# Performance work log

Hardware: AMD Instinct MI355X
Metric: run time of the kernel (lower is better)

The kernel has to match this reference:

```python
import jax, jax.numpy as jnp
import numpy as np

L = 1024   # latent_size
K = 8
R = L // K # 128 reduced dim
T = 32     # caption length
B = 64     # batch (images and captions)
DIN = 300  # word embedding dim
REG = 36   # image regions
R3 = 3 * R
H3 = 3 * L

def _p(key, shape, scale=0.05):
    return scale * jax.random.normal(key, shape, dtype=jnp.float32)

def setup_inputs():
    ks = jax.random.split(jax.random.key(0), 40)
    return {
        'img_embed': jax.random.normal(ks[0], (B, REG, L), jnp.float32),
        'cap_embed': jax.random.normal(ks[1], (B, T, DIN), jnp.float32),
        'lens': jax.random.randint(ks[2], (B,), 1, T + 1),
        'W_reduce_img': _p(ks[3], (R, L)), 'b_reduce_img': _p(ks[4], (R,)),
        'W_reduce_txt': _p(ks[5], (R, DIN)), 'b_reduce_txt': _p(ks[6], (R,)),
        'gru_Wih_f': _p(ks[7], (H3, DIN)), 'gru_Whh_f': _p(ks[8], (H3, L)),
        'gru_bih_f': _p(ks[9], (H3,)), 'gru_bhh_f': _p(ks[10], (H3,)),
        'gru_Wih_b': _p(ks[11], (H3, DIN)), 'gru_Whh_b': _p(ks[12], (H3, L)),
        'gru_bih_b': _p(ks[13], (H3,)), 'gru_bhh_b': _p(ks[14], (H3,)),
        'sa_Wq': _p(ks[15], (R, L)), 'sa_bq': _p(ks[16], (R,)),
        'sa_Wk': _p(ks[17], (R, L)), 'sa_bk': _p(ks[18], (R,)),
        'sa_Wv': _p(ks[19], (L, L)), 'sa_bv': _p(ks[20], (L,)),
        'sa_gamma': jnp.float32(0.5),
        'gen_Wih': _p(ks[21], (R3 * R, R)), 'gen_bih': _p(ks[22], (R3 * R,)),
        'gen_Whh': _p(ks[23], (R3 * R, R)), 'gen_bhh': _p(ks[24], (R3 * R,)),
        'gen_Wbih': _p(ks[25], (R3, R)), 'gen_bbih': _p(ks[26], (R3,)),
        'gen_Wbhh': _p(ks[27], (R3, R)), 'gen_bbhh': _p(ks[28], (R3,)),
        'W_txt_fc': _p(ks[29], (L, R + L)), 'b_txt_fc': _p(ks[30], (L,)),
    }

def l2norm(x, axis=-1, eps=1e-8):
    return x / (jnp.linalg.norm(x, axis=axis, keepdims=True) + eps)

def gru_dir(x, Wih, Whh, bih, bhh, reverse=False):
    # torch GRU math, gate order [r, z, n]; x: (B, T, D) -> (B, T, H)
    H = Whh.shape[1]
    gi = jnp.einsum('btd,hd->tbh', x, Wih) + bih  # precompute input gates (T, B, 3H)
    h0 = jnp.zeros((x.shape[0], H), x.dtype)
    def step(h, gi_t):
        gh = h @ Whh.T + bhh
        r = jax.nn.sigmoid(gi_t[:, :H] + gh[:, :H])
        z = jax.nn.sigmoid(gi_t[:, H:2 * H] + gh[:, H:2 * H])
        n = jnp.tanh(gi_t[:, 2 * H:] + r * gh[:, 2 * H:])
        hn = (1.0 - z) * n + z * h
        return hn, hn
    _, hs = jax.lax.scan(step, h0, gi, reverse=reverse)
    return jnp.swapaxes(hs, 0, 1)

def _forward(img_embed, cap_embed, lens, W_reduce_img, b_reduce_img, W_reduce_txt, b_reduce_txt,
             gru_Wih_f, gru_Whh_f, gru_bih_f, gru_bhh_f, gru_Wih_b, gru_Whh_b, gru_bih_b, gru_bhh_b,
             sa_Wq, sa_bq, sa_Wk, sa_bk, sa_Wv, sa_bv, sa_gamma,
             gen_Wih, gen_bih, gen_Whh, gen_bhh, gen_Wbih, gen_bbih, gen_Wbhh, gen_bbhh,
             W_txt_fc, b_txt_fc):
    # 1. bidirectional GRU over captions, average the two directions
    hf = gru_dir(cap_embed, gru_Wih_f, gru_Whh_f, gru_bih_f, gru_bhh_f, False)
    hb = gru_dir(cap_embed, gru_Wih_b, gru_Whh_b, gru_bih_b, gru_bhh_b, True)
    txt = (hf + hb) / 2.0                                   # (B, T, L)
    # 2. SAGAN-style 1D self-attention on (B, L, T)
    x = jnp.swapaxes(txt, 1, 2)                             # (B, L, T)
    q = jnp.einsum('bct,oc->bto', x, sa_Wq) + sa_bq          # (B, T, R)
    kk = jnp.einsum('bct,oc->bot', x, sa_Wk) + sa_bk[:, None]  # (B, R, T)
    attn = jax.nn.softmax(jnp.einsum('bto,bos->bts', q, kk), axis=-1)  # (B, T, T)
    v = jnp.einsum('bct,oc->bot', x, sa_Wv) + sa_bv[:, None]  # (B, L, T)
    x = sa_gamma * jnp.einsum('bcs,bts->bct', v, attn) + x
    # 3. length-masked mean pooling
    txt = jnp.swapaxes(x, 1, 2)                             # (B, T, L)
    mask = (jnp.arange(T)[None, :] < lens[:, None]).astype(txt.dtype)
    txt_embed = (txt * mask[:, :, None]).sum(1) / lens[:, None].astype(txt.dtype)  # (B, L)
    # 4. conv1d(k=1) reductions == linear over channel dim
    img = jnp.swapaxes(img_embed, 1, 2)                     # (B, L, REG)
    img_embed_global = img.mean(-1)                         # (B, L)
    cap_reduced = jnp.einsum('btd,od->btd2'.replace('d2','o'), cap_embed, W_reduce_txt) + b_reduce_txt  # (B, T, R)
    img_reduced = jnp.einsum('bcr,oc->bor', img, W_reduce_img) + b_reduce_img[:, None]  # (B, R, REG)
    img_global_vec = img_reduced.mean(-1)                   # (B, R)
    # 5. per-image generated-weight GRU over all captions (vmap replaces B-loop)
    def per_image(base, img_glob):
        Wih = (gen_Wih @ base + gen_bih).reshape(R3, R)
        Whh = (gen_Whh @ base + gen_bhh).reshape(R3, R)
        bih = gen_Wbih @ base + gen_bbih
        bhh = gen_Wbhh @ base + gen_bbhh
        gi = jnp.einsum('btd,hd->tbh', cap_reduced, Wih) + bih  # (T, B, 3R)
        h0 = jnp.zeros((cap_reduced.shape[0], R), cap_reduced.dtype)
        def step(h, gi_t):
            gh = h @ Whh.T + bhh
            r = jax.nn.sigmoid(gi_t[:, :R] + gh[:, :R])
            z = jax.nn.sigmoid(gi_t[:, R:2 * R] + gh[:, R:2 * R])
            n = jnp.tanh(gi_t[:, 2 * R:] + r * gh[:, 2 * R:])
            hn = (1.0 - z) * n + z * h
            return hn, hn
        _, hs = jax.lax.scan(step, h0, gi)                  # (T, B, R)
        txt_vec = hs.max(0)                                 # max over time -> (B, R)
        txt_vec = jnp.concatenate([txt_embed, txt_vec], axis=1) @ W_txt_fc.T + b_txt_fc
        txt_vec = l2norm(txt_vec)                           # (B, L)
        iv = l2norm(img_glob)                               # (L,)
        return txt_vec @ iv                                 # (B,) cosine sims for this image
    sims = jax.vmap(per_image)(img_global_vec, img_embed_global)  # (B_img, B_cap)
    return sims

def reference(img_embed, cap_embed, lens, W_reduce_img, b_reduce_img, W_reduce_txt, b_reduce_txt,
              gru_Wih_f, gru_Whh_f, gru_bih_f, gru_bhh_f, gru_Wih_b, gru_Whh_b, gru_bih_b, gru_bhh_b,
              sa_Wq, sa_bq, sa_Wk, sa_bk, sa_Wv, sa_bv, sa_gamma,
              gen_Wih, gen_bih, gen_Whh, gen_bhh, gen_Wbih, gen_bbih, gen_Wbhh, gen_bbhh,
              W_txt_fc, b_txt_fc):
    return _forward(img_embed, cap_embed, lens, W_reduce_img, b_reduce_img, W_reduce_txt, b_reduce_txt,
                    gru_Wih_f, gru_Whh_f, gru_bih_f, gru_bhh_f, gru_Wih_b, gru_Whh_b, gru_bih_b, gru_bhh_b,
                    sa_Wq, sa_bq, sa_Wk, sa_bk, sa_Wv, sa_bv, sa_gamma,
                    gen_Wih, gen_bih, gen_Whh, gen_bhh, gen_Wbih, gen_bbih, gen_Wbhh, gen_bbhh,
                    W_txt_fc, b_txt_fc)
```

## Files before the change

kernel.cpp:

```cpp
#include <hip/hip_runtime.h>
#include <math.h>

#define Lsz   1024
#define Tsz   32
#define Bsz   64
#define DIN   300
#define REG   36
#define Rsz   128
#define R3sz  384
#define H3sz  3072
#define GENROWS 49152
#define NC    2048
#define KPAD  304

typedef __attribute__((ext_vector_type(8))) short bf16x8;
typedef __attribute__((ext_vector_type(4))) float f32x4;

__device__ __forceinline__ float sigf(float x) { return 1.f / (1.f + __expf(-x)); }

__device__ __forceinline__ ushort f2bf(float x) {
    unsigned u = __float_as_uint(x);
    unsigned r = (u + 0x7fffu + ((u >> 16) & 1u)) >> 16;
    return (ushort)r;
}
// ... 311 lines not shown
    int ctp = blockIdx.x;
    int col = ctp * 16 + (l & 15);
    int kb = kt * 32 + (l >> 4) * 8;
    float v[8];
#pragma unroll
    for (int e = 0; e < 8; e++)
        v[e] = capT2[(size_t)(kb + e) * NC + col];
    size_t off = ((size_t)kt * 128 + ctp) * 512 + l * 8;
    pack8(v, (ushort*)CFh_ + off, (ushort*)CFl_ + off);
}

__global__ __launch_bounds__(256) void packwih_kernel(
    const float* __restrict__ Wf, const float* __restrict__ Wb,
    float* __restrict__ Fh, float* __restrict__ Fl)
{
    int tid = threadIdx.x, l = tid & 63, wid = tid >> 6;
    int kt = blockIdx.x * 4 + wid;
    int m = blockIdx.y, dir = blockIdx.z;
    if (kt >= 10) return;
    const float* W = dir ? Wb : Wf;
    int row = m * 16 + (l & 15);
    int kb = kt * 32 + (l >> 4) * 8;
    float v[8];
#pragma unroll
    for (int e = 0; e < 8; e++) {
        int k = kb + e;
        v[e] = (k < DIN) ? W[(size_t)row * DIN + k] : 0.f;
    }
    size_t off = (((size_t)dir * 192 + m) * 10 + kt) * 512 + l * 8;
    pack8(v, (ushort*)Fh + off, (ushort*)Fl + off);
}

__global__ __launch_bounds__(256) void packcapb_kernel(
    const float* __restrict__ cap_embed, float* __restrict__ Fh, float* __restrict__ Fl)
{
    int tid = threadIdx.x, l = tid & 63, wid = tid >> 6;
    int ct = blockIdx.x;
    int kt = blockIdx.y * 4 + wid;
    if (kt >= 10) return;
    int c = ct * 16 + (l & 15), t = c >> 6, b = c & 63;
    int kb = kt * 32 + (l >> 4) * 8;
    float v[8];
#pragma unroll
    for (int e = 0; e < 8; e++) {
        int k = kb + e;
        v[e] = (k < DIN) ? cap_embed[((size_t)b * Tsz + t) * DIN + k] : 0.f;
    }
    size_t off = ((size_t)kt * 128 + ct) * 512 + l * 8;
    pack8(v, (ushort*)Fh + off, (ushort*)Fl + off);
}

__global__ __launch_bounds__(256) void packA_rm(
    const float* __restrict__ W, float* __restrict__ Fh, float* __restrict__ Fl,
    int lda, int koff, int NKT)
{
    int tid = threadIdx.x, l = tid & 63, wid = tid >> 6;
    int strip = blockIdx.x;
    int kt = blockIdx.y * 4 + wid;
    if (kt >= NKT) return;
    int row = strip * 16 + (l & 15);
    int kb = kt * 32 + (l >> 4) * 8;
    float v[8];
    *(float4*)&v[0] = *(const float4*)&W[(size_t)row * lda + koff + kb];
    *(float4*)&v[4] = *(const float4*)&W[(size_t)row * lda + koff + kb + 4];
    size_t off = ((size_t)strip * NKT + kt) * 512 + l * 8;
    pack8(v, (ushort*)Fh + off, (ushort*)Fl + off);
}

__global__ __launch_bounds__(256) void packB_kernel(
    const float* __restrict__ X, float* __restrict__ Fh, float* __restrict__ Fl,
    int ncols, int NKT)
{
    int tid = threadIdx.x, l = tid & 63, wid = tid >> 6;
    int ctp = blockIdx.x;
    int kt = blockIdx.y * 4 + wid;
    if (kt >= NKT) return;
    int col = ctp * 16 + (l & 15);
    int kb = kt * 32 + (l >> 4) * 8;
    float v[8];
#pragma unroll
    for (int e = 0; e < 8; e++)
        v[e] = X[(size_t)(kb + e) * ncols + col];
    size_t off = ((size_t)kt * (ncols >> 4) + ctp) * 512 + l * 8;
    pack8(v, (ushort*)Fh + off, (ushort*)Fl + off);
}

__global__ __launch_bounds__(256) void gemm_mfma(
    const float* __restrict__ AFh, const float* __restrict__ AFl,
    const float* __restrict__ BFh, const float* __restrict__ BFl,
    const float* __restrict__ bias, float* __restrict__ C,
    int NKT, int ncols)
{
    __shared__ __align__(16) ushort BsH[8][512];
    __shared__ __align__(16) ushort BsL[8][512];
    int tid = threadIdx.x, l = tid & 63, wid = tid >> 6;
    int ctg = blockIdx.x, mg = blockIdx.y;
    int ct0 = ctg * 8;
    int m0 = mg * 8 + wid * 2;
    int nct = ncols >> 4;
    const ushort* AH = (const ushort*)AFh;
    const ushort* AL = (const ushort*)AFl;
    const ushort* BH = (const ushort*)BFh;
    const ushort* BL = (const ushort*)BFl;

    f32x4 acc[2][8];
#pragma unroll
    for (int m = 0; m < 2; m++)
#pragma unroll
        for (int ct = 0; ct < 8; ct++) acc[m][ct] = (f32x4){0.f, 0.f, 0.f, 0.f};

    for (int kt = 0; kt < NKT; kt++) {
        __syncthreads();
#pragma unroll
        for (int u = 0; u < 2; u++) {
            int e = u * 256 + tid;
            int ct = e >> 6, p8 = (e & 63) * 8;
            *(uint4*)&BsH[ct][p8] = *(const uint4*)&BH[((size_t)kt * nct + ct0 + ct) * 512 + p8];
            *(uint4*)&BsL[ct][p8] = *(const uint4*)&BL[((size_t)kt * nct + ct0 + ct) * 512 + p8];
        }
        __syncthreads();
        bf16x8 Ah[2], Al[2];
#pragma unroll
        for (int m = 0; m < 2; m++) {
            size_t ao = ((size_t)(m0 + m) * NKT + kt) * 512 + l * 8;
            Ah[m] = *(const bf16x8*)(AH + ao);
            Al[m] = *(const bf16x8*)(AL + ao);
        }
#pragma unroll
        for (int ct = 0; ct < 8; ct++) {
            bf16x8 Bh = *(const bf16x8*)&BsH[ct][l * 8];
            bf16x8 Bl = *(const bf16x8*)&BsL[ct][l * 8];
#pragma unroll
            for (int m = 0; m < 2; m++) {
                acc[m][ct] = __builtin_amdgcn_mfma_f32_16x16x32_bf16(Ah[m], Bh, acc[m][ct], 0, 0, 0);
                acc[m][ct] = __builtin_amdgcn_mfma_f32_16x16x32_bf16(Ah[m], Bl, acc[m][ct], 0, 0, 0);
                acc[m][ct] = __builtin_amdgcn_mfma_f32_16x16x32_bf16(Al[m], Bh, acc[m][ct], 0, 0, 0);
            }
        }
    }
    int row4 = (l >> 4) * 4, col = l & 15;
#pragma unroll
    for (int m = 0; m < 2; m++) {
        int nb_ = (m0 + m) * 16 + row4;
#pragma unroll
        for (int r = 0; r < 4; r++) {
            float bv = bias ? bias[nb_ + r] : 0.f;
#pragma unroll
            for (int ct = 0; ct < 8; ct++)
                C[(size_t)(nb_ + r) * ncols + (size_t)(ct0 + ct) * 16 + col] = acc[m][ct][r] + bv;
        }
    }
}

__global__ __launch_bounds__(256) void rec_kernel(
    const float* __restrict__ WhhF_h, const float* __restrict__ WhhF_l,
    const float* __restrict__ WgenF_h, const float* __restrict__ WgenF_l,
    const float* __restrict__ capF_h, const float* __restrict__ capF_l,
    float* capHF_h, float* capHF_l,
    float* genHF_h, float* genHF_l,
    const float* __restrict__ giT2_f, const float* __restrict__ giT2_b,
    float* hfT, float* hbT,
    const float* __restrict__ bhh_f, const float* __restrict__ bhh_b,
    const float* __restrict__ bihAll, const float* __restrict__ bhhAll,
    float* hA, float* hB, float* hmaxT,
    int s)
{
    __shared__ float red[48 * 256];
    int tid = threadIdx.x, l = tid & 63, wid = tid >> 6;
    int bid = blockIdx.x;
    int ping = (s & 1) ^ 1;
    int pong = s & 1;

    if (bid < 128) {
        int dir = bid >> 6, js = bid & 63;
        f32x4 acc[3][4];
#pragma unroll
        for (int g = 0; g < 3; g++)
#pragma unroll
            for (int ct = 0; ct < 4; ct++) acc[g][ct] = (f32x4){0.f, 0.f, 0.f, 0.f};

        if (s > 0) {
            const ushort* Wh = (const ushort*)WhhF_h + (size_t)dir * (192 * 32 * 512);
            const ushort* Wl = (const ushort*)WhhF_l + (size_t)dir * (192 * 32 * 512);
            const ushort* Hh = (const ushort*)capHF_h + (size_t)(dir * 2 + ping) * 65536;
            const ushort* Hl = (const ushort*)capHF_l + (size_t)(dir * 2 + ping) * 65536;
            for (int k8 = 0; k8 < 8; k8++) {
                int k0 = wid * 8 + k8;
                bf16x8 Bh[4], Bl[4], Ah[3], Al[3];
#pragma unroll
                for (int ct = 0; ct < 4; ct++) {
                    size_t fo = ((size_t)k0 * 4 + ct) * 512 + l * 8;
                    Bh[ct] = *(const bf16x8*)(Hh + fo);
                    Bl[ct] = *(const bf16x8*)(Hl + fo);
                }
#pragma unroll
                for (int g = 0; g < 3; g++) {
                    size_t fo = ((size_t)(g * 64 + js) * 32 + k0) * 512 + l * 8;
                    Ah[g] = *(const bf16x8*)(Wh + fo);
                    Al[g] = *(const bf16x8*)(Wl + fo);
                }
#pragma unroll
                for (int g = 0; g < 3; g++)
#pragma unroll
                    for (int ct = 0; ct < 4; ct++)
                        acc[g][ct] = __builtin_amdgcn_mfma_f32_16x16x32_bf16(
                            Ah[g], Bh[ct], acc[g][ct], 0, 0, 0);
#pragma unroll
                for (int g = 0; g < 3; g++)
#pragma unroll
                    for (int ct = 0; ct < 4; ct++)
                        acc[g][ct] = __builtin_amdgcn_mfma_f32_16x16x32_bf16(
                            Ah[g], Bl[ct], acc[g][ct], 0, 0, 0);
#pragma unroll
                for (int g = 0; g < 3; g++)
#pragma unroll
                    for (int ct = 0; ct < 4; ct++)
                        acc[g][ct] = __builtin_amdgcn_mfma_f32_16x16x32_bf16(
                            Al[g], Bh[ct], acc[g][ct], 0, 0, 0);
            }
        }
#pragma unroll
        for (int g = 0; g < 3; g++)
#pragma unroll
            for (int ct = 0; ct < 4; ct++)
                *(f32x4*)&red[((wid * 3 + g) * 4 + ct) * 256 + l * 4] = acc[g][ct];
        __syncthreads();

        const float* giT = dir ? giT2_b : giT2_f;
        float* hT        = dir ? hbT   : hfT;
        const float* bhh = dir ? bhh_b : bhh_f;
        int t  = dir ? (Tsz - 1 - s) : s;
        int tp = dir ? (t + 1) : (t - 1);
        ushort* Ch = (ushort*)capHF_h + (size_t)(dir * 2 + pong) * 65536;
        ushort* Cl = (ushort*)capHF_l + (size_t)(dir * 2 + pong) * 65536;
#pragma unroll
        for (int u = 0; u < 4; u++) {
            int e = u * 256 + tid;
            int jj = e >> 6, b = e & 63;
            int j = js * 16 + jj;
            float gh[3] = {0.f, 0.f, 0.f};
            if (s > 0) {
                int lane_ = ((jj >> 2) << 4) | (b & 15);
                int reg = jj & 3, ct = b >> 4;
#pragma unroll
                for (int w = 0; w < 4; w++)
#pragma unroll
                    for (int g = 0; g < 3; g++)
                        gh[g] += red[((w * 3 + g) * 4 + ct) * 256 + lane_ * 4 + reg];
            }
            size_t gc = (size_t)t * 64 + b;
            float gr = giT[(size_t)j * NC + gc];
            float gz = giT[((size_t)Lsz + j) * NC + gc];
            float gn = giT[((size_t)2 * Lsz + j) * NC + gc];
            float hp = (s > 0) ? hT[((size_t)tp * Lsz + j) * Bsz + b] : 0.f;
            float r = sigf(gr + gh[0] + bhh[j]);
            float z = sigf(gz + gh[1] + bhh[Lsz + j]);
            float n = tanhf(gn + r * (gh[2] + bhh[2 * Lsz + j]));
            float h = (1.f - z) * n + z * hp;
            hT[((size_t)t * Lsz + j) * Bsz + b] = h;
            size_t fo = hfrag_off(j, b);
            ushort hb = f2bf(h);
            Ch[fo] = hb;
            Cl[fo] = f2bf(h - bf2f(hb));
        }
    } else {
        int g2 = bid - 128;
        int i = g2 >> 2;
        int p = g2 & 3;
        int mat = wid & 1;
        int sl = wid >> 1;
        int strip = p * 2 + sl;
        float* hcurT = (s & 1) ? hB : hA;
        const float* hprevT = (s & 1) ? hA : hB;
        f32x4 acc[3][4];
#pragma unroll
        for (int g = 0; g < 3; g++)
#pragma unroll
            for (int ct = 0; ct < 4; ct++) acc[g][ct] = (f32x4){0.f, 0.f, 0.f, 0.f};

        if (mat == 0 || s > 0) {
            const ushort* Ahp = (const ushort*)WgenF_h + (size_t)(i * 2 + mat) * 96 * 512;
            const ushort* Alp = (const ushort*)WgenF_l + (size_t)(i * 2 + mat) * 96 * 512;
            const ushort* Bhp;
            const ushort* Blp;
            if (mat == 0) {
                Bhp = (const ushort*)capF_h;
                Blp = (const ushort*)capF_l;
            } else {
                Bhp = (const ushort*)genHF_h + (size_t)(ping * 64 + i) * 8192;
                Blp = (const ushort*)genHF_l + (size_t)(ping * 64 + i) * 8192;
            }
            for (int kt = 0; kt < 4; kt++) {
                bf16x8 Bh[4], Bl[4], Ah[3], Al[3];
#pragma unroll
                for (int ct = 0; ct < 4; ct++) {
                    size_t fo = (mat == 0)
                        ? ((size_t)kt * 128 + s * 4 + ct) * 512 + l * 8
                        : ((size_t)kt * 4 + ct) * 512 + l * 8;
                    Bh[ct] = *(const bf16x8*)(Bhp + fo);
                    Bl[ct] = *(const bf16x8*)(Blp + fo);
                }
#pragma unroll
                for (int g = 0; g < 3; g++) {
                    size_t fo = ((size_t)(g * 8 + strip) * 4 + kt) * 512 + l * 8;
                    Ah[g] = *(const bf16x8*)(Ahp + fo);
                    Al[g] = *(const bf16x8*)(Alp + fo);
                }
#pragma unroll
                for (int g = 0; g < 3; g++)
#pragma unroll
                    for (int ct = 0; ct < 4; ct++)
                        acc[g][ct] = __builtin_amdgcn_mfma_f32_16x16x32_bf16(
                            Ah[g], Bh[ct], acc[g][ct], 0, 0, 0);
#pragma unroll
                for (int g = 0; g < 3; g++)
#pragma unroll
                    for (int ct = 0; ct < 4; ct++)
                        acc[g][ct] = __builtin_amdgcn_mfma_f32_16x16x32_bf16(
                            Ah[g], Bl[ct], acc[g][ct], 0, 0, 0);
#pragma unroll
                for (int g = 0; g < 3; g++)
#pragma unroll
                    for (int ct = 0; ct < 4; ct++)
                        acc[g][ct] = __builtin_amdgcn_mfma_f32_16x16x32_bf16(
                            Al[g], Bh[ct], acc[g][ct], 0, 0, 0);
            }
        }
#pragma unroll
        for (int g = 0; g < 3; g++)
#pragma unroll
            for (int ct = 0; ct < 4; ct++)
                *(f32x4*)&red[(((sl * 2 + mat) * 3 + g) * 4 + ct) * 256 + l * 4] = acc[g][ct];
        __syncthreads();

        const float* bih = bihAll + (size_t)i * R3sz;
        const float* bhh = bhhAll + (size_t)i * R3sz;
        ushort* Gh = (ushort*)genHF_h + (size_t)(pong * 64 + i) * 8192;
        ushort* Gl = (ushort*)genHF_l + (size_t)(pong * 64 + i) * 8192;
#pragma unroll
        for (int u = 0; u < 8; u++) {
            int e = u * 256 + tid;
            int sl2 = e >> 10;
            int jj = (e >> 6) & 15;
            int b = e & 63;
            int j = (p * 2 + sl2) * 16 + jj;
            int lane_ = ((jj >> 2) << 4) | (b & 15);
            int reg = jj & 3, ct = b >> 4;
            float sih[3], shh[3];
#pragma unroll
            for (int g = 0; g < 3; g++) {
                sih[g] = red[(((sl2 * 2 + 0) * 3 + g) * 4 + ct) * 256 + lane_ * 4 + reg];
                shh[g] = (s > 0)
                    ? red[(((sl2 * 2 + 1) * 3 + g) * 4 + ct) * 256 + lane_ * 4 + reg]
                    : 0.f;
            }
            float r = sigf(sih[0] + bih[j] + shh[0] + bhh[j]);
            float z = sigf(sih[1] + bih[Rsz + j] + shh[1] + bhh[Rsz + j]);
            float n = tanhf(sih[2] + bih[2 * Rsz + j] + r * (shh[2] + bhh[2 * Rsz + j]));
            float hp = (s > 0) ? hprevT[((size_t)i * Rsz + j) * Bsz + b] : 0.f;
            float h = (1.f - z) * n + z * hp;
            size_t idx = ((size_t)i * Rsz + j) * Bsz + b;
            hcurT[idx] = h;
            hmaxT[idx] = (s == 0) ? h : fmaxf(hmaxT[idx], h);
            size_t fo = hfrag_off(j, b);
            ushort hb = f2bf(h);
            Gh[fo] = hb;
            Gl[fo] = f2bf(h - bf2f(hb));
        }
    }
}

__global__ __launch_bounds__(256) void txt_combine(
    const float* __restrict__ hfT, const float* __restrict__ hbT,
    float* __restrict__ txt, float* __restrict__ txtT)
{
    __shared__ float s[64][65];
    int t = blockIdx.x;
    int c0 = blockIdx.y * 64;
    int tid = threadIdx.x;
#pragma unroll
    for (int l = 0; l < 16; l++) {
        int e = l * 256 + tid;
        int cc = e >> 6, b = e & 63;
        size_t idx = ((size_t)t * Lsz + c0 + cc) * Bsz + b;
        s[cc][b] = 0.5f * (hfT[idx] + hbT[idx]);
    }
    __syncthreads();
#pragma unroll
    for (int l = 0; l < 16; l++) {
        int e = l * 256 + tid;
        int b = e >> 6, cc = e & 63;
        txt[((size_t)b * Tsz + t) * Lsz + c0 + cc] = s[cc][b];
    }
#pragma unroll
    for (int l = 0; l < 16; l++) {
        int e = l * 256 + tid;
        int cc = e >> 6, b = e & 63;
        txtT[(size_t)(c0 + cc) * NC + t * 64 + b] = s[cc][b];
    }
}

__global__ __launch_bounds__(256) void attn_kernel(
    const float* __restrict__ q, const float* __restrict__ kmat,
    const float* __restrict__ vbuf,
    const float* __restrict__ txt,
    const float* __restrict__ gamma_p, float* __restrict__ xattn)
{
    __shared__ float qs[32][129];
    __shared__ float ks[32][129];
    __shared__ float Sc[32][33];
    __shared__ float vs[128][33];
    int b = blockIdx.x;
    int c0 = blockIdx.y * 128;
    int tid = threadIdx.x;
    for (int e = tid; e < Tsz * Rsz; e += 256) {
        qs[e >> 7][e & 127] = q[(size_t)b * Tsz * Rsz + e];
        ks[e >> 7][e & 127] = kmat[(size_t)b * Tsz * Rsz + e];
    }
    for (int e = tid; e < 128 * 32; e += 256) {
        int cc = e >> 5, ss = e & 31;
        vs[cc][ss] = vbuf[(size_t)(c0 + cc) * NC + ss * 64 + b];
    }
    __syncthreads();
    for (int e = tid; e < Tsz * Tsz; e += 256) {
        int t = e >> 5, ss = e & 31;
        float acc = 0.f;
#pragma unroll 4
        for (int o = 0; o < Rsz; o++) acc = fmaf(qs[t][o], ks[ss][o], acc);
        Sc[t][ss] = acc;
    }
    __syncthreads();
    if (tid < 32) {
        int t = tid;
        float mx = -1e30f;
#pragma unroll
        for (int ss = 0; ss < 32; ss++) mx = fmaxf(mx, Sc[t][ss]);
        float sum = 0.f;
        float ex[32];
#pragma unroll
        for (int ss = 0; ss < 32; ss++) { ex[ss] = __expf(Sc[t][ss] - mx); sum += ex[ss]; }
        float inv = 1.f / sum;
#pragma unroll
        for (int ss = 0; ss < 32; ss++) Sc[t][ss] = ex[ss] * inv;
    }
    __syncthreads();
    float gamma = *gamma_p;
    for (int e = tid; e < Tsz * 128; e += 256) {
        int tt = e >> 7, cc = e & 127;
        float acc = 0.f;
#pragma unroll 8
        for (int ss = 0; ss < Tsz; ss++)
            acc = fmaf(Sc[tt][ss], vs[cc][ss], acc);
        size_t oidx = ((size_t)b * Tsz + tt) * Lsz + c0 + cc;
        xattn[oidx] = gamma * acc + txt[oidx];
    }
}

__global__ __launch_bounds__(256) void pool_kernel(
    const float* __restrict__ xattn, const int* __restrict__ lens,
    float* __restrict__ txt_embed)
{
    int b = blockIdx.x;
    int c = blockIdx.y * 256 + threadIdx.x;
    int len = lens[b];
    float s = 0.f;
    for (int t = 0; t < len; t++) s += xattn[((size_t)b * Tsz + t) * Lsz + c];
    txt_embed[(size_t)b * Lsz + c] = s / (float)len;
}

__global__ __launch_bounds__(256) void basefc_kernel(
    const float* __restrict__ temb, const float* __restrict__ W,
    float* __restrict__ outT)
{
    int lane = threadIdx.x & 63, w = threadIdx.x >> 6;
    int n = blockIdx.x * 4 + w;
    const float* wr = W + (size_t)n * (Rsz + Lsz) + lane * 16;
    float wv[16];
#pragma unroll
    for (int u = 0; u < 4; u++) *(float4*)&wv[u * 4] = *(const float4*)&wr[u * 4];
    for (int b = 0; b < Bsz; b++) {
        const float* te = temb + (size_t)b * Lsz + lane * 16;
        float tv[16];
#pragma unroll
        for (int u = 0; u < 4; u++) *(float4*)&tv[u * 4] = *(const float4*)&te[u * 4];
        float a = 0.f;
#pragma unroll
        for (int u = 0; u < 16; u++) a = fmaf(wv[u], tv[u], a);
#pragma unroll
        for (int off = 32; off; off >>= 1) a += __shfl_down(a, off, 64);
        if (lane == 0) outT[(size_t)n * Bsz + b] = a;
    }
}

__global__ __launch_bounds__(256) void hstdT_kernel(
    const float* __restrict__ hmaxT, float* __restrict__ hstdT)
{
    int i = blockIdx.x, tid = threadIdx.x;
    int b = tid & 63, j0 = tid >> 6;
#pragma unroll
    for (int l = 0; l < 32; l++) {
        int j = l * 4 + j0;
        hstdT[(size_t)j * 4096 + i * 64 + b] = hmaxT[((size_t)i * Rsz + j) * Bsz + b];
    }
}

__global__ __launch_bounds__(256) void sims_part(
    const float* __restrict__ fcT, const float* __restrict__ base_fcT,
    const float* __restrict__ bfc, const float* __restrict__ iv,
    float* __restrict__ accA, float* __restrict__ accB)
{
    int i = blockIdx.x, cs = blockIdx.y;
    int tid = threadIdx.x;
    int w = tid >> 6, b = tid & 63;
    float s1 = 0.f, s2 = 0.f;
    for (int u = 0; u < 64; u++) {
        int c = cs * 256 + w * 64 + u;
        float f = fcT[(size_t)c * 4096 + i * 64 + b] + base_fcT[(size_t)c * Bsz + b] + bfc[c];
        s1 = fmaf(f, f, s1);
        s2 = fmaf(f, iv[(size_t)i * Lsz + c], s2);
    }
    int m = i * 64 + b;
    atomicAdd(&accA[m], s1);
    atomicAdd(&accB[m], s2);
}

__global__ __launch_bounds__(256) void sims_final(
    const float* __restrict__ accA, const float* __restrict__ accB,
    float* __restrict__ out)
{
    int m = blockIdx.x * 256 + threadIdx.x;
    out[m] = accB[m] / (sqrtf(accA[m]) + 1e-8f);
}

extern "C" void kernel_launch(void* const* d_in, const int* in_sizes, int n_in,
                              void* d_out, int out_size, void* d_ws, size_t ws_size,
                              hipStream_t stream)
{
    const float* img_embed    = (const float*)d_in[0];
    const float* cap_embed    = (const float*)d_in[1];
    const int*   lens         = (const int*)d_in[2];
    const float* W_reduce_img = (const float*)d_in[3];
    const float* b_reduce_img = (const float*)d_in[4];
    const float* W_reduce_txt = (const float*)d_in[5];
    const float* b_reduce_txt = (const float*)d_in[6];
    const float* gru_Wih_f    = (const float*)d_in[7];
    const float* gru_Whh_f    = (const float*)d_in[8];
    const float* gru_bih_f    = (const float*)d_in[9];
    const float* gru_bhh_f    = (const float*)d_in[10];
    const float* gru_Wih_b    = (const float*)d_in[11];
    const float* gru_Whh_b    = (const float*)d_in[12];
    const float* gru_bih_b    = (const float*)d_in[13];
    const float* gru_bhh_b    = (const float*)d_in[14];
    const float* sa_Wq        = (const float*)d_in[15];
    const float* sa_bq        = (const float*)d_in[16];
    const float* sa_Wk        = (const float*)d_in[17];
    const float* sa_bk        = (const float*)d_in[18];
    const float* sa_Wv        = (const float*)d_in[19];
    const float* sa_bv        = (const float*)d_in[20];
    const float* sa_gamma     = (const float*)d_in[21];
    const float* gen_Wih      = (const float*)d_in[22];
    const float* gen_bih      = (const float*)d_in[23];
    const float* gen_Whh      = (const float*)d_in[24];
    const float* gen_bhh      = (const float*)d_in[25];
    const float* gen_Wbih     = (const float*)d_in[26];
    const float* gen_bbih     = (const float*)d_in[27];
    const float* gen_Wbhh     = (const float*)d_in[28];
    const float* gen_bbhh     = (const float*)d_in[29];
    const float* W_txt_fc     = (const float*)d_in[30];
    const float* b_txt_fc     = (const float*)d_in[31];

    float* ws = (float*)d_ws;
    size_t off = 0;
    auto alloc = [&](size_t n) { float* p = ws + off; off += n; return p; };
    float* giT2_f   = alloc((size_t)H3sz * NC);
    float* giT2_b   = alloc((size_t)H3sz * NC);
    float* hfT      = alloc((size_t)Tsz * Lsz * Bsz);
    float* hbT      = alloc((size_t)Tsz * Lsz * Bsz);
    float* capTr    = alloc((size_t)KPAD * NC);
    float* capT2    = alloc((size_t)Rsz * NC);
    float* txt      = alloc((size_t)Bsz * Tsz * Lsz);
    float* txtT     = alloc((size_t)Lsz * NC);
    float* qbuf     = alloc((size_t)Bsz * Tsz * Rsz);
    float* kbuf     = alloc((size_t)Bsz * Tsz * Rsz);
    float* pool     = alloc((size_t)12582912);
    float* WhhFh  = pool;
    float* WhhFl  = pool + 3145728;
    float* WgenFh = pool + 6291456;
    float* WgenFl = pool + 9437184;
    float* txtFh  = pool;
    float* txtFl  = pool + 1048576;
    float* hstdFh = pool + 2097152;
    float* hstdFl = pool + 2359296;
    float* vbuf   = pool + 2621440;
    float* qkbuf  = pool + 4718592;
    float* fcT    = pool + 5242880;
    float* xattn    = alloc((size_t)Bsz * Tsz * Lsz);
    float* txt_emb  = alloc((size_t)Bsz * Lsz);
    float* base     = alloc((size_t)Bsz * Rsz);
    float* iv       = alloc((size_t)Bsz * Lsz);
    float* WihAllT  = alloc((size_t)Bsz * GENROWS);
    float* WhhAllT  = alloc((size_t)Bsz * GENROWS);
    float* WihFh    = alloc((size_t)983040);
    float* WihFl    = alloc((size_t)983040);
    float* capBFh   = alloc((size_t)327680);
    float* capBFl   = alloc((size_t)327680);
    float* WvFh     = alloc((size_t)524288);
    float* WvFl     = alloc((size_t)524288);
    float* WqkFh    = alloc((size_t)131072);
    float* WqkFl    = alloc((size_t)131072);
    float* WfcFh    = alloc((size_t)65536);
    float* WfcFl    = alloc((size_t)65536);
    float* WrtT     = alloc((size_t)KPAD * Rsz);
    float* bihAll   = alloc((size_t)Bsz * R3sz);
    float* bhhAll   = alloc((size_t)Bsz * R3sz);
    float* hA       = alloc((size_t)Bsz * Rsz * Bsz);
    float* hB       = alloc((size_t)Bsz * Rsz * Bsz);
    float* hmaxT    = alloc((size_t)Bsz * Rsz * Bsz);
    float* hstdT    = alloc((size_t)Rsz * Bsz * Bsz);
    float* base_fcT = alloc((size_t)Lsz * Bsz);
    float* accA     = alloc(4096);
    float* accB     = alloc(4096);
    float* capFh    = alloc(131072);
    float* capFl    = alloc(131072);
    float* capHFh   = alloc(131072);
    float* capHFl   = alloc(131072);
    float* genHFh   = alloc(524288);
    float* genHFl   = alloc(524288);

    hipMemsetAsync(accA, 0, 2 * 4096 * sizeof(float), stream);

    transp_kernel<<<dim3(5, 2), 256, 0, stream>>>(W_reduce_txt, WrtT, Rsz, DIN, KPAD, DIN, 0);
    captr_kernel<<<dim3(32, 5), 256, 0, stream>>>(cap_embed, capTr);
    packwih_kernel<<<dim3(3, 192, 2), 256, 0, stream>>>(gru_Wih_f, gru_Wih_b, WihFh, WihFl);
    packcapb_kernel<<<dim3(128, 3), 256, 0, stream>>>(cap_embed, capBFh, capBFl);
    packA_rm<<<dim3(64, 8), 256, 0, stream>>>(sa_Wv, WvFh, WvFl, Lsz, 0, 32);
    packA_rm<<<dim3(8, 8), 256, 0, stream>>>(sa_Wq, WqkFh, WqkFl, Lsz, 0, 32);
    packA_rm<<<dim3(8, 8), 256, 0, stream>>>(sa_Wk, WqkFh + 65536, WqkFl + 65536, Lsz, 0, 32);
    packA_rm<<<dim3(64, 1), 256, 0, stream>>>(W_txt_fc, WfcFh, WfcFl, Rsz + Lsz, Lsz, 4);

    img_kernel<<<64, 256, 0, stream>>>(img_embed, W_reduce_img, b_reduce_img, base, iv);
    genw_gemm<<<dim3(3, 129, 2), 256, 0, stream>>>(gen_Wih, gen_bih, gen_Whh, gen_bhh,
        gen_Wbih, gen_bbih, gen_Wbhh, gen_bbhh, base, WihAllT, WhhAllT, bihAll, bhhAll);
    packwhh_kernel<<<dim3(8, 192, 2), 256, 0, stream>>>(gru_Whh_f, gru_Whh_b, WhhFh, WhhFl);
    packgenw_kernel<<<dim3(24, 2, 64), 256, 0, stream>>>(WihAllT, WhhAllT, WgenFh, WgenFl);

    gemm_mfma<<<dim3(16, 24), 256, 0, stream>>>(WihFh, WihFl, capBFh, capBFl,
        gru_bih_f, giT2_f, 10, NC);
    gemm_mfma<<<dim3(16, 24), 256, 0, stream>>>(WihFh + 491520, WihFl + 491520,
        capBFh, capBFl, gru_bih_b, giT2_b, 10, NC);
    gemm_tt<<<dim3(16, 1, 1), 256, 0, stream>>>(WrtT, WrtT, capTr,
        b_reduce_txt, b_reduce_txt, capT2, capT2, Rsz);
    packcap_kernel<<<128, 256, 0, stream>>>(capT2, capFh, capFl);

    for (int s = 0; s < Tsz; s++) {
        rec_kernel<<<384, 256, 0, stream>>>(WhhFh, WhhFl, WgenFh, WgenFl,
            capFh, capFl, capHFh, capHFl, genHFh, genHFl, giT2_f, giT2_b,
            hfT, hbT, gru_bhh_f, gru_bhh_b, bihAll, bhhAll, hA, hB, hmaxT, s);
    }
    hstdT_kernel<<<64, 256, 0, stream>>>(hmaxT, hstdT);

    txt_combine<<<dim3(32, 16), 256, 0, stream>>>(hfT, hbT, txt, txtT);
    packB_kernel<<<dim3(128, 8), 256, 0, stream>>>(txtT, txtFh, txtFl, NC, 32);
    packB_kernel<<<dim3(256, 1), 256, 0, stream>>>(hstdT, hstdFh, hstdFl, 4096, 4);
    gemm_mfma<<<dim3(16, 2), 256, 0, stream>>>(WqkFh, WqkFl, txtFh, txtFl,
        nullptr, qkbuf, 32, NC);
    gemm_mfma<<<dim3(16, 8), 256, 0, stream>>>(WvFh, WvFl, txtFh, txtFl,
        sa_bv, vbuf, 32, NC);
    qkc_kernel<<<dim3(32, 2), 256, 0, stream>>>(qkbuf, sa_bq, sa_bk, qbuf, kbuf);
    attn_kernel<<<dim3(64, 8), 256, 0, stream>>>(qbuf, kbuf, vbuf, txt,
        sa_gamma, xattn);

    pool_kernel<<<dim3(64, 4), 256, 0, stream>>>(xattn, lens, txt_emb);
    basefc_kernel<<<256, 256, 0, stream>>>(txt_emb, W_txt_fc, base_fcT);

    gemm_mfma<<<dim3(32, 8), 256, 0, stream>>>(WfcFh, WfcFl, hstdFh, hstdFl,
        nullptr, fcT, 4, 4096);
    sims_part<<<dim3(64, 4), 256, 0, stream>>>(fcT, base_fcT, b_txt_fc, iv, accA, accB);
    sims_final<<<16, 256, 0, stream>>>(accA, accB, (float*)d_out);
}
```

Before: 1.261 ms.

## Fuse 32 recurrence launches into one persistent kernel with flag sync

Replaces the per-timestep launch loop of the recurrence kernel with a single persistent kernel that loops over timesteps internally. Blocks coordinate through per-step, per-group flags in global memory, using acquire loads in a spin-wait and release stores after a threadfence. Each GRU direction waits on all 64 blocks of its own direction, and each generated-GRU group waits on its 4 partner blocks. This removes launch overhead and the device-wide barrier between steps, but it depends on all 384 blocks being co-resident and adds spin-polling cost.

```diff
diff --git a/kernel.cpp b/kernel.cpp
--- a/kernel.cpp
+++ b/kernel.cpp
@@ -487,7 +487,7 @@
     }
 }
 
-__global__ __launch_bounds__(256) void rec_kernel(
+__global__ __launch_bounds__(256) void rec_all(
     const float* __restrict__ WhhF_h, const float* __restrict__ WhhF_l,
     const float* __restrict__ WgenF_h, const float* __restrict__ WgenF_l,
     const float* __restrict__ capF_h, const float* __restrict__ capF_l,
@@ -498,105 +498,123 @@
     const float* __restrict__ bhh_f, const float* __restrict__ bhh_b,
     const float* __restrict__ bihAll, const float* __restrict__ bhhAll,
     float* hA, float* hB, float* hmaxT,
-    int s)
+    unsigned* flags)
 {
     __shared__ float red[48 * 256];
     int tid = threadIdx.x, l = tid & 63, wid = tid >> 6;
     int bid = blockIdx.x;
-    int ping = (s & 1) ^ 1;
-    int pong = s & 1;
+    unsigned* capf = flags;
+    unsigned* genf = flags + 4096;
 
     if (bid < 128) {
         int dir = bid >> 6, js = bid & 63;
-        f32x4 acc[3][4];
-#pragma unroll
-        for (int g = 0; g < 3; g++)
-#pragma unroll
-            for (int ct = 0; ct < 4; ct++) acc[g][ct] = (f32x4){0.f, 0.f, 0.f, 0.f};
-
-        if (s > 0) {
-            const ushort* Wh = (const ushort*)WhhF_h + (size_t)dir * (192 * 32 * 512);
-            const ushort* Wl = (const ushort*)WhhF_l + (size_t)dir * (192 * 32 * 512);
-            const ushort* Hh = (const ushort*)capHF_h + (size_t)(dir * 2 + ping) * 65536;
-            const ushort* Hl = (const ushort*)capHF_l + (size_t)(dir * 2 + ping) * 65536;
-            for (int k8 = 0; k8 < 8; k8++) {
-                int k0 = wid * 8 + k8;
-                bf16x8 Bh[4], Bl[4], Ah[3], Al[3];
-#pragma unroll
-                for (int ct = 0; ct < 4; ct++) {
-                    size_t fo = ((size_t)k0 * 4 + ct) * 512 + l * 8;
-                    Bh[ct] = *(const bf16x8*)(Hh + fo);
-                    Bl[ct] = *(const bf16x8*)(Hl + fo);
-                }
-#pragma unroll
-                for (int g = 0; g < 3; g++) {
-                    size_t fo = ((size_t)(g * 64 + js) * 32 + k0) * 512 + l * 8;
-                    Ah[g] = *(const bf16x8*)(Wh + fo);
-                    Al[g] = *(const bf16x8*)(Wl + fo);
-                }
-#pragma unroll
-                for (int g = 0; g < 3; g++)
-#pragma unroll
-                    for (int ct = 0; ct < 4; ct++)
-                        acc[g][ct] = __builtin_amdgcn_mfma_f32_16x16x32_bf16(
-                            Ah[g], Bh[ct], acc[g][ct], 0, 0, 0);
-#pragma unroll
-                for (int g = 0; g < 3; g++)
-#pragma unroll
-                    for (int ct = 0; ct < 4; ct++)
-                        acc[g][ct] = __builtin_amdgcn_mfma_f32_16x16x32_bf16(
-                            Ah[g], Bl[ct], acc[g][ct], 0, 0, 0);
-#pragma unroll
-                for (int g = 0; g < 3; g++)
-#pragma unroll
-                    for (int ct = 0; ct < 4; ct++)
-                        acc[g][ct] = __builtin_amdgcn_mfma_f32_16x16x32_bf16(
-                            Al[g], Bh[ct], acc[g][ct], 0, 0, 0);
-            }
-        }
-#pragma unroll
-        for (int g = 0; g < 3; g++)
-#pragma unroll
-            for (int ct = 0; ct < 4; ct++)
-                *(f32x4*)&red[((wid * 3 + g) * 4 + ct) * 256 + l * 4] = acc[g][ct];
-        __syncthreads();
-
         const float* giT = dir ? giT2_b : giT2_f;
         float* hT        = dir ? hbT   : hfT;
         const float* bhh = dir ? bhh_b : bhh_f;
-        int t  = dir ? (Tsz - 1 - s) : s;
-        int tp = dir ? (t + 1) : (t - 1);
-        ushort* Ch = (ushort*)capHF_h + (size_t)(dir * 2 + pong) * 65536;
-        ushort* Cl = (ushort*)capHF_l + (size_t)(dir * 2 + pong) * 65536;
-#pragma unroll
-        for (int u = 0; u < 4; u++) {
-            int e = u * 256 + tid;
-            int jj = e >> 6, b = e & 63;
-            int j = js * 16 + jj;
-            float gh[3] = {0.f, 0.f, 0.f};
+        const ushort* Wh = (const ushort*)WhhF_h + (size_t)dir * (192 * 32 * 512);
+        const ushort* Wl = (const ushort*)WhhF_l + (size_t)dir * (192 * 32 * 512);
+        unsigned* myf = capf + dir * 2048;
+
+        for (int s = 0; s < Tsz; ++s) {
+            int ping = (s & 1) ^ 1, pong = s & 1;
+            f32x4 acc[3][4];
+#pragma unroll
+            for (int g = 0; g < 3; g++)
+#pragma unroll
+                for (int ct = 0; ct < 4; ct++) acc[g][ct] = (f32x4){0.f, 0.f, 0.f, 0.f};
+
             if (s > 0) {
-                int lane_ = ((jj >> 2) << 4) | (b & 15);
-                int reg = jj & 3, ct = b >> 4;
-#pragma unroll
-                for (int w = 0; w < 4; w++)
+                if (tid < 64) {
+                    const unsigned* f = myf + (s - 1) * 64 + tid;
+                    while (!__all(__hip_atomic_load(f, __ATOMIC_ACQUIRE,
+                                                    __HIP_MEMORY_SCOPE_AGENT) != 0u))
+                        __builtin_amdgcn_s_sleep(8);
+                }
+                __syncthreads();
+
+                const ushort* Hh = (const ushort*)capHF_h + (size_t)(dir * 2 + ping) * 65536;
+                const ushort* Hl = (const ushort*)capHF_l + (size_t)(dir * 2 + ping) * 65536;
+                for (int k8 = 0; k8 < 8; k8++) {
+                    int k0 = wid * 8 + k8;
+                    bf16x8 Bh[4], Bl[4], Ah[3], Al[3];
+#pragma unroll
+                    for (int ct = 0; ct < 4; ct++) {
+                        size_t fo = ((size_t)k0 * 4 + ct) * 512 + l * 8;
+                        Bh[ct] = *(const bf16x8*)(Hh + fo);
+                        Bl[ct] = *(const bf16x8*)(Hl + fo);
+                    }
+#pragma unroll
+                    for (int g = 0; g < 3; g++) {
+                        size_t fo = ((size_t)(g * 64 + js) * 32 + k0) * 512 + l * 8;
+                        Ah[g] = *(const bf16x8*)(Wh + fo);
+                        Al[g] = *(const bf16x8*)(Wl + fo);
+                    }
 #pragma unroll
                     for (int g = 0; g < 3; g++)
-                        gh[g] += red[((w * 3 + g) * 4 + ct) * 256 + lane_ * 4 + reg];
+#pragma unroll
+                        for (int ct = 0; ct < 4; ct++)
+                            acc[g][ct] = __builtin_amdgcn_mfma_f32_16x16x32_bf16(
+                                Ah[g], Bh[ct], acc[g][ct], 0, 0, 0);
+#pragma unroll
+                    for (int g = 0; g < 3; g++)
+#pragma unroll
+                        for (int ct = 0; ct < 4; ct++)
+                            acc[g][ct] = __builtin_amdgcn_mfma_f32_16x16x32_bf16(
+                                Ah[g], Bl[ct], acc[g][ct], 0, 0, 0);
+#pragma unroll
+                    for (int g = 0; g < 3; g++)
+#pragma unroll
+                        for (int ct = 0; ct < 4; ct++)
+                            acc[g][ct] = __builtin_amdgcn_mfma_f32_16x16x32_bf16(
+                                Al[g], Bh[ct], acc[g][ct], 0, 0, 0);
+                }
             }
-            size_t gc = (size_t)t * 64 + b;
-            float gr = giT[(size_t)j * NC + gc];
-            float gz = giT[((size_t)Lsz + j) * NC + gc];
-            float gn = giT[((size_t)2 * Lsz + j) * NC + gc];
-            float hp = (s > 0) ? hT[((size_t)tp * Lsz + j) * Bsz + b] : 0.f;
-            float r = sigf(gr + gh[0] + bhh[j]);
-            float z = sigf(gz + gh[1] + bhh[Lsz + j]);
-            float n = tanhf(gn + r * (gh[2] + bhh[2 * Lsz + j]));
-            float h = (1.f - z) * n + z * hp;
-            hT[((size_t)t * Lsz + j) * Bsz + b] = h;
-            size_t fo = hfrag_off(j, b);
-            ushort hb = f2bf(h);
-            Ch[fo] = hb;
-            Cl[fo] = f2bf(h - bf2f(hb));
+#pragma unroll
+            for (int g = 0; g < 3; g++)
+#pragma unroll
+                for (int ct = 0; ct < 4; ct++)
+                    *(f32x4*)&red[((wid * 3 + g) * 4 + ct) * 256 + l * 4] = acc[g][ct];
+            __syncthreads();
+
+            int t  = dir ? (Tsz - 1 - s) : s;
+            int tp = dir ? (t + 1) : (t - 1);
+            ushort* Ch = (ushort*)capHF_h + (size_t)(dir * 2 + pong) * 65536;
+            ushort* Cl = (ushort*)capHF_l + (size_t)(dir * 2 + pong) * 65536;
+#pragma unroll
+            for (int u = 0; u < 4; u++) {
+                int e = u * 256 + tid;
+                int jj = e >> 6, b = e & 63;
+                int j = js * 16 + jj;
+                float gh[3] = {0.f, 0.f, 0.f};
+                if (s > 0) {
+                    int lane_ = ((jj >> 2) << 4) | (b & 15);
+                    int reg = jj & 3, ct = b >> 4;
+#pragma unroll
+                    for (int w = 0; w < 4; w++)
+#pragma unroll
+                        for (int g = 0; g < 3; g++)
+                            gh[g] += red[((w * 3 + g) * 4 + ct) * 256 + lane_ * 4 + reg];
+                }
+                size_t gc = (size_t)t * 64 + b;
+                float gr = giT[(size_t)j * NC + gc];
+                float gz = giT[((size_t)Lsz + j) * NC + gc];
+                float gn = giT[((size_t)2 * Lsz + j) * NC + gc];
+                float hp = (s > 0) ? hT[((size_t)tp * Lsz + j) * Bsz + b] : 0.f;
+                float r = sigf(gr + gh[0] + bhh[j]);
+                float z = sigf(gz + gh[1] + bhh[Lsz + j]);
+                float n = tanhf(gn + r * (gh[2] + bhh[2 * Lsz + j]));
+                float h = (1.f - z) * n + z * hp;
+                hT[((size_t)t * Lsz + j) * Bsz + b] = h;
+                size_t fo = hfrag_off(j, b);
+                ushort hb = f2bf(h);
+                Ch[fo] = hb;
+                Cl[fo] = f2bf(h - bf2f(hb));
+            }
+            __threadfence();
+            __syncthreads();
+            if (tid == 0)
+                __hip_atomic_store(myf + s * 64 + js, 1u, __ATOMIC_RELEASE,
+                                   __HIP_MEMORY_SCOPE_AGENT);
         }
     } else {
         int g2 = bid - 128;
@@ -605,102 +623,122 @@
         int mat = wid & 1;
         int sl = wid >> 1;
         int strip = p * 2 + sl;
-        float* hcurT = (s & 1) ? hB : hA;
-        const float* hprevT = (s & 1) ? hA : hB;
-        f32x4 acc[3][4];
-#pragma unroll
-        for (int g = 0; g < 3; g++)
-#pragma unroll
-            for (int ct = 0; ct < 4; ct++) acc[g][ct] = (f32x4){0.f, 0.f, 0.f, 0.f};
-
-        if (mat == 0 || s > 0) {
-            const ushort* Ahp = (const ushort*)WgenF_h + (size_t)(i * 2 + mat) * 96 * 512;
-            const ushort* Alp = (const ushort*)WgenF_l + (size_t)(i * 2 + mat) * 96 * 512;
-            const ushort* Bhp;
-            const ushort* Blp;
-            if (mat == 0) {
-                Bhp = (const ushort*)capF_h;
-                Blp = (const ushort*)capF_l;
-            } else {
-                Bhp = (const ushort*)genHF_h + (size_t)(ping * 64 + i) * 8192;
-                Blp = (const ushort*)genHF_l + (size_t)(ping * 64 + i) * 8192;
-            }
-            for (int kt = 0; kt < 4; kt++) {
-                bf16x8 Bh[4], Bl[4], Ah[3], Al[3];
-#pragma unroll
-                for (int ct = 0; ct < 4; ct++) {
-                    size_t fo = (mat == 0)
-                        ? ((size_t)kt * 128 + s * 4 + ct) * 512 + l * 8
-                        : ((size_t)kt * 4 + ct) * 512 + l * 8;
-                    Bh[ct] = *(const bf16x8*)(Bhp + fo);
-                    Bl[ct] = *(const bf16x8*)(Blp + fo);
-                }
-#pragma unroll
-                for (int g = 0; g < 3; g++) {
-                    size_t fo = ((size_t)(g * 8 + strip) * 4 + kt) * 512 + l * 8;
-                    Ah[g] = *(const bf16x8*)(Ahp + fo);
-                    Al[g] = *(const bf16x8*)(Alp + fo);
-                }
-#pragma unroll
-                for (int g = 0; g < 3; g++)
-#pragma unroll
-                    for (int ct = 0; ct < 4; ct++)
-                        acc[g][ct] = __builtin_amdgcn_mfma_f32_16x16x32_bf16(
-                            Ah[g], Bh[ct], acc[g][ct], 0, 0, 0);
-#pragma unroll
-                for (int g = 0; g < 3; g++)
-#pragma unroll
-                    for (int ct = 0; ct < 4; ct++)
-                        acc[g][ct] = __builtin_amdgcn_mfma_f32_16x16x32_bf16(
-                            Ah[g], Bl[ct], acc[g][ct], 0, 0, 0);
-#pragma unroll
-                for (int g = 0; g < 3; g++)
-#pragma unroll
-                    for (int ct = 0; ct < 4; ct++)
-                        acc[g][ct] = __builtin_amdgcn_mfma_f32_16x16x32_bf16(
-                            Al[g], Bh[ct], acc[g][ct], 0, 0, 0);
-            }
-        }
-#pragma unroll
-        for (int g = 0; g < 3; g++)
-#pragma unroll
-            for (int ct = 0; ct < 4; ct++)
-                *(f32x4*)&red[(((sl * 2 + mat) * 3 + g) * 4 + ct) * 256 + l * 4] = acc[g][ct];
-        __syncthreads();
-
         const float* bih = bihAll + (size_t)i * R3sz;
         const float* bhh = bhhAll + (size_t)i * R3sz;
-        ushort* Gh = (ushort*)genHF_h + (size_t)(pong * 64 + i) * 8192;
-        ushort* Gl = (ushort*)genHF_l + (size_t)(pong * 64 + i) * 8192;
-#pragma unroll
-        for (int u = 0; u < 8; u++) {
-            int e = u * 256 + tid;
-            int sl2 = e >> 10;
-            int jj = (e >> 6) & 15;
-            int b = e & 63;
-            int j = (p * 2 + sl2) * 16 + jj;
-            int lane_ = ((jj >> 2) << 4) | (b & 15);
-            int reg = jj & 3, ct = b >> 4;
-            float sih[3], shh[3];
-#pragma unroll
-            for (int g = 0; g < 3; g++) {
-                sih[g] = red[(((sl2 * 2 + 0) * 3 + g) * 4 + ct) * 256 + lane_ * 4 + reg];
-                shh[g] = (s > 0)
-                    ? red[(((sl2 * 2 + 1) * 3 + g) * 4 + ct) * 256 + lane_ * 4 + reg]
-                    : 0.f;
+        const ushort* Ahp = (const ushort*)WgenF_h + (size_t)(i * 2 + mat) * 96 * 512;
+        const ushort* Alp = (const ushort*)WgenF_l + (size_t)(i * 2 + mat) * 96 * 512;
+        unsigned* myf = genf + i * 128;
+
+        for (int s = 0; s < Tsz; ++s) {
+            int ping = (s & 1) ^ 1, pong = s & 1;
+            float* hcurT = (s & 1) ? hB : hA;
+            const float* hprevT = (s & 1) ? hA : hB;
+            f32x4 acc[3][4];
+#pragma unroll
+            for (int g = 0; g < 3; g++)
+#pragma unroll
+                for (int ct = 0; ct < 4; ct++) acc[g][ct] = (f32x4){0.f, 0.f, 0.f, 0.f};
+
+            if (s > 0) {
+                if (tid < 4) {
+                    const unsigned* f = myf + (s - 1) * 4 + tid;
+                    while (!__all(__hip_atomic_load(f, __ATOMIC_ACQUIRE,
+                                                    __HIP_MEMORY_SCOPE_AGENT) != 0u))
+                        __builtin_amdgcn_s_sleep(8);
+                }
+                __syncthreads();
             }
-            float r = sigf(sih[0] + bih[j] + shh[0] + bhh[j]);
-            float z = sigf(sih[1] + bih[Rsz + j] + shh[1] + bhh[Rsz + j]);
-            float n = tanhf(sih[2] + bih[2 * Rsz + j] + r * (shh[2] + bhh[2 * Rsz + j]));
-            float hp = (s > 0) ? hprevT[((size_t)i * Rsz + j) * Bsz + b] : 0.f;
-            float h = (1.f - z) * n + z * hp;
-            size_t idx = ((size_t)i * Rsz + j) * Bsz + b;
-            hcurT[idx] = h;
-            hmaxT[idx] = (s == 0) ? h : fmaxf(hmaxT[idx], h);
-            size_t fo = hfrag_off(j, b);
-            ushort hb = f2bf(h);
-            Gh[fo] = hb;
-            Gl[fo] = f2bf(h - bf2f(hb));
+
+            if (mat == 0 || s > 0) {
+                const ushort* Bhp;
+                const ushort* Blp;
+                if (mat == 0) {
+                    Bhp = (const ushort*)capF_h;
+                    Blp = (const ushort*)capF_l;
+                } else {
+                    Bhp = (const ushort*)genHF_h + (size_t)(ping * 64 + i) * 8192;
+                    Blp = (const ushort*)genHF_l + (size_t)(ping * 64 + i) * 8192;
+                }
+                for (int kt = 0; kt < 4; kt++) {
+                    bf16x8 Bh[4], Bl[4], Ah[3], Al[3];
+#pragma unroll
+                    for (int ct = 0; ct < 4; ct++) {
+                        size_t fo = (mat == 0)
+                            ? ((size_t)kt * 128 + s * 4 + ct) * 512 + l * 8
+                            : ((size_t)kt * 4 + ct) * 512 + l * 8;
+                        Bh[ct] = *(const bf16x8*)(Bhp + fo);
+                        Bl[ct] = *(const bf16x8*)(Blp + fo);
+                    }
+#pragma unroll
+                    for (int g = 0; g < 3; g++) {
+                        size_t fo = ((size_t)(g * 8 + strip) * 4 + kt) * 512 + l * 8;
+                        Ah[g] = *(const bf16x8*)(Ahp + fo);
+                        Al[g] = *(const bf16x8*)(Alp + fo);
+                    }
+#pragma unroll
+                    for (int g = 0; g < 3; g++)
+#pragma unroll
+                        for (int ct = 0; ct < 4; ct++)
+                            acc[g][ct] = __builtin_amdgcn_mfma_f32_16x16x32_bf16(
+                                Ah[g], Bh[ct], acc[g][ct], 0, 0, 0);
+#pragma unroll
+                    for (int g = 0; g < 3; g++)
+#pragma unroll
+                        for (int ct = 0; ct < 4; ct++)
+                            acc[g][ct] = __builtin_amdgcn_mfma_f32_16x16x32_bf16(
+                                Ah[g], Bl[ct], acc[g][ct], 0, 0, 0);
+#pragma unroll
+                    for (int g = 0; g < 3; g++)
+#pragma unroll
+                        for (int ct = 0; ct < 4; ct++)
+                            acc[g][ct] = __builtin_amdgcn_mfma_f32_16x16x32_bf16(
+                                Al[g], Bh[ct], acc[g][ct], 0, 0, 0);
+                }
+            }
+#pragma unroll
+            for (int g = 0; g < 3; g++)
+#pragma unroll
+                for (int ct = 0; ct < 4; ct++)
+                    *(f32x4*)&red[(((sl * 2 + mat) * 3 + g) * 4 + ct) * 256 + l * 4] = acc[g][ct];
+            __syncthreads();
+
+            ushort* Gh = (ushort*)genHF_h + (size_t)(pong * 64 + i) * 8192;
+            ushort* Gl = (ushort*)genHF_l + (size_t)(pong * 64 + i) * 8192;
+#pragma unroll
+            for (int u = 0; u < 8; u++) {
+                int e = u * 256 + tid;
+                int sl2 = e >> 10;
+                int jj = (e >> 6) & 15;
+                int b = e & 63;
+                int j = (p * 2 + sl2) * 16 + jj;
+                int lane_ = ((jj >> 2) << 4) | (b & 15);
+                int reg = jj & 3, ct = b >> 4;
+                float sih[3], shh[3];
+#pragma unroll
+                for (int g = 0; g < 3; g++) {
+                    sih[g] = red[(((sl2 * 2 + 0) * 3 + g) * 4 + ct) * 256 + lane_ * 4 + reg];
+                    shh[g] = (s > 0)
+                        ? red[(((sl2 * 2 + 1) * 3 + g) * 4 + ct) * 256 + lane_ * 4 + reg]
+                        : 0.f;
+                }
+                float r = sigf(sih[0] + bih[j] + shh[0] + bhh[j]);
+                float z = sigf(sih[1] + bih[Rsz + j] + shh[1] + bhh[Rsz + j]);
+                float n = tanhf(sih[2] + bih[2 * Rsz + j] + r * (shh[2] + bhh[2 * Rsz + j]));
+                float hp = (s > 0) ? hprevT[((size_t)i * Rsz + j) * Bsz + b] : 0.f;
+                float h = (1.f - z) * n + z * hp;
+                size_t idx = ((size_t)i * Rsz + j) * Bsz + b;
+                hcurT[idx] = h;
+                hmaxT[idx] = (s == 0) ? h : fmaxf(hmaxT[idx], h);
+                size_t fo = hfrag_off(j, b);
+                ushort hb = f2bf(h);
+                Gh[fo] = hb;
+                Gl[fo] = f2bf(h - bf2f(hb));
+            }
+            __threadfence();
+            __syncthreads();
+            if (tid == 0)
+                __hip_atomic_store(myf + s * 4 + p, 1u, __ATOMIC_RELEASE,
+                                   __HIP_MEMORY_SCOPE_AGENT);
         }
     }
 }
@@ -961,8 +999,10 @@
     float* capHFl   = alloc(131072);
     float* genHFh   = alloc(524288);
     float* genHFl   = alloc(524288);
+    float* flags    = alloc(12288);
 
     hipMemsetAsync(accA, 0, 2 * 4096 * sizeof(float), stream);
+    hipMemsetAsync(flags, 0, 12288 * sizeof(float), stream);
 
     transp_kernel<<<dim3(5, 2), 256, 0, stream>>>(W_reduce_txt, WrtT, Rsz, DIN, KPAD, DIN, 0);
     captr_kernel<<<dim3(32, 5), 256, 0, stream>>>(cap_embed, capTr);
@@ -987,11 +1027,10 @@
         b_reduce_txt, b_reduce_txt, capT2, capT2, Rsz);
     packcap_kernel<<<128, 256, 0, stream>>>(capT2, capFh, capFl);
 
-    for (int s = 0; s < Tsz; s++) {
-        rec_kernel<<<384, 256, 0, stream>>>(WhhFh, WhhFl, WgenFh, WgenFl,
-            capFh, capFl, capHFh, capHFl, genHFh, genHFl, giT2_f, giT2_b,
-            hfT, hbT, gru_bhh_f, gru_bhh_b, bihAll, bhhAll, hA, hB, hmaxT, s);
-    }
+    rec_all<<<384, 256, 0, stream>>>(WhhFh, WhhFl, WgenFh, WgenFl,
+        capFh, capFl, capHFh, capHFl, genHFh, genHFl, giT2_f, giT2_b,
+        hfT, hbT, gru_bhh_f, gru_bhh_b, bihAll, bhhAll, hA, hB, hmaxT,
+        (unsigned*)flags);
     hstdT_kernel<<<64, 256, 0, stream>>>(hmaxT, hstdT);
 
     txt_combine<<<dim3(32, 16), 256, 0, stream>>>(hfT, hbT, txt, txtT);
```

After: 3.479 ms. 2.76x slower.
